# Kernel tuning notes

Hardware: AMD Instinct MI355X
Metric: run time of the kernel (lower is better)

Reference implementation:

```python
import jax, jax.numpy as jnp
import numpy as np

N = 50000          # nodes
E_RAW = 600000     # edges before self loops
FEAT = 64
HID = 64
HEADS = 4
NUM_SUBST = 32
NUM_GRAPHS = 128


def setup_inputs() -> dict:
    key = jax.random.key(0)
    ks = jax.random.split(key, 24)
    s = 0.05
    x = jax.random.normal(ks[0], (N, FEAT), jnp.float32)
    sids = jax.random.randint(ks[1], (N,), 0, NUM_SUBST)
    x = x.at[:, 5].set(sids.astype(jnp.float32))  # x[:,5] holds integer substructure ids
    edge_index = jax.random.randint(ks[2], (2, E_RAW), 0, N, dtype=jnp.int32)
    batch = jnp.sort(jax.random.randint(ks[3], (N,), 0, NUM_GRAPHS, dtype=jnp.int32))
    p = lambda i, shape: jax.random.normal(ks[i], shape, jnp.float32) * s
    return dict(
        x=x, edge_index=edge_index, batch=batch,
        # substructure attention MLP: Linear(FEAT,32) -> LeakyReLU(0.2) -> Linear(32,1)
        w_sa1=p(4, (FEAT, 32)), b_sa1=p(5, (32,)),
        w_sa2=p(6, (32, 1)), b_sa2=p(7, (1,)),
        # GATConv 1: in=FEAT+1, out=HID, heads=HEADS, concat
        W1=p(8, (FEAT + 1, HEADS * HID)), att_s1=p(9, (HEADS, HID)),
        att_d1=p(10, (HEADS, HID)), b1=p(11, (HEADS * HID,)),
        # GATConv 2: in=HEADS*HID, out=HID, heads=1
        W2=p(12, (HEADS * HID, HID)), att_s2=p(13, (1, HID)),
        att_d2=p(14, (1, HID)), b2=p(15, (HID,)),
        # prediction head
        Wp1=p(16, (HID, HID // 2)), bp1=p(17, (HID // 2,)),
        Wp2=p(18, (HID // 2, 1)), bp2=p(19, (1,)),
    )


def _gat_layer(h_in, src, dst, W, att_s, att_d, bias, n):
    heads, out_dim = att_s.shape
    h = (h_in @ W).reshape(n, heads, out_dim)            # [N, H, D]
    a_s = jnp.einsum('nhd,hd->nh', h, att_s)             # [N, H]
    a_d = jnp.einsum('nhd,hd->nh', h, att_d)
    e = jax.nn.leaky_relu(a_s[src] + a_d[dst], negative_slope=0.2)  # [E, H]
    m = jax.ops.segment_max(e, dst, num_segments=n)
    ex = jnp.exp(e - m[dst])
    denom = jax.ops.segment_sum(ex, dst, num_segments=n)
    alpha = ex / (denom[dst] + 1e-16)                    # segment softmax per dst node
    out = jax.ops.segment_sum(h[src] * alpha[..., None], dst, num_segments=n)
    return out.reshape(n, heads * out_dim) + bias        # concat heads + bias


def reference(x, edge_index, batch, w_sa1, b_sa1, w_sa2, b_sa2,
              W1, att_s1, att_d1, b1, W2, att_s2, att_d2, b2,
              Wp1, bp1, Wp2, bp2):
    n = x.shape[0]
    sid = jax.lax.stop_gradient(x[:, 5]).astype(jnp.int32)
    # segment mean of node features per substructure id (all NUM_SUBST ids present)
    cnt = jax.ops.segment_sum(jnp.ones((n,), x.dtype), sid, num_segments=NUM_SUBST)
    smean = jax.ops.segment_sum(x, sid, num_segments=NUM_SUBST) / jnp.maximum(cnt, 1.0)[:, None]
    logits = jax.nn.leaky_relu(smean @ w_sa1 + b_sa1, negative_slope=0.2) @ w_sa2 + b_sa2
    w = jax.nn.softmax(logits, axis=0)                   # [S, 1]
    atom_w = w[sid]                                      # broadcast back to atoms [N, 1]
    h = jnp.concatenate([x, atom_w], axis=1)             # [N, FEAT+1]
    # add_self_loops (gat2's remove+add self loops yields the same edge set)
    loops = jnp.arange(n, dtype=edge_index.dtype)
    src = jnp.concatenate([edge_index[0], loops])
    dst = jnp.concatenate([edge_index[1], loops])
    h = jax.nn.elu(_gat_layer(h, src, dst, W1, att_s1, att_d1, b1, n))
    h = _gat_layer(h, src, dst, W2, att_s2, att_d2, b2, n)
    g = jax.ops.segment_sum(h, batch, num_segments=NUM_GRAPHS)   # global_add_pool
    return jax.nn.elu(g @ Wp1 + bp1) @ Wp2 + bp2         # [NUM_GRAPHS, 1]
```

## Files before the change

### kernel.cpp

```cpp
#include <hip/hip_runtime.h>
#include <math.h>

#define N_NODES 50000
#define E_RAWN  600000
#define FEAT    64
#define HID     64
#define HEADS   4
#define NSUB    32
#define NGRAPH  128
#define NB_SCAN ((N_NODES + 255) / 256)
#define G2_NODES 128

__device__ __forceinline__ float leaky02(float v) { return v >= 0.f ? v : 0.2f * v; }
__device__ __forceinline__ float elu1(float v)    { return v > 0.f ? v : expm1f(v); }

__device__ __forceinline__ unsigned bf2pack(float a, float b) {
    unsigned ua = __float_as_uint(a), ub = __float_as_uint(b);
    ua = (ua + 0x7FFFu + ((ua >> 16) & 1u)) >> 16;
    ub = (ub + 0x7FFFu + ((ub >> 16) & 1u)) >> 16;
    return ua | (ub << 16);
}
__device__ __forceinline__ float bflo(unsigned p) { return __uint_as_float(p << 16); }
__device__ __forceinline__ float bfhi(unsigned p) { return __uint_as_float(p & 0xFFFF0000u); }
__device__ __forceinline__ float bfs(unsigned short v) { return __uint_as_float((unsigned)v << 16); }

__global__ void k_prep(const float* __restrict__ x,
                       float* __restrict__ ssum, float* __restrict__ scnt,
                       const int* __restrict__ dst, int* __restrict__ cnt) {
    int tid = threadIdx.x;
    if (blockIdx.x < 256) {
        __shared__ float lsum[NSUB * FEAT];
        __shared__ float lcnt[NSUB];
        for (int i = tid; i < NSUB * FEAT; i += 256) lsum[i] = 0.f;
        if (tid < NSUB) lcnt[tid] = 0.f;
        __syncthreads();
        const int total = N_NODES * FEAT;
        for (int idx = blockIdx.x * 256 + tid; idx < total; idx += 256 * 256) {
            int node = idx >> 6, f = idx & 63;
            int sid = (int)x[node * FEAT + 5];
            atomicAdd(&lsum[sid * FEAT + f], x[idx]);
            if (f == 0) atomicAdd(&lcnt[sid], 1.f);
        }
        __syncthreads();
        for (int i = tid; i < NSUB * FEAT; i += 256) atomicAdd(&ssum[i], lsum[i]);
        if (tid < NSUB) atomicAdd(&scnt[tid], lcnt[tid]);
    } else {
        for (int e = (blockIdx.x - 256) * 256 + tid; e < E_RAWN; e += 256 * 256)
            atomicAdd(&cnt[dst[e]], 1);
    }
}

__global__ void k_mlp_scan1(const int* __restrict__ cnt, int* __restrict__ offs, int* __restrict__ bsum,
                            const float* __restrict__ ssum, const float* __restrict__ scnt,
                            const float* __restrict__ w_sa1, const float* __restrict__ b_sa1,
                            const float* __restrict__ w_sa2, const float* __restrict__ b_sa2,
                            float* __restrict__ wsub) {
    int tid = threadIdx.x;
    if (blockIdx.x == NB_SCAN) {
        __shared__ float logits[NSUB];
        int s = tid;
        if (s < NSUB) {
            float c = fmaxf(scnt[s], 1.f);
            float sm[FEAT];
            for (int k = 0; k < FEAT; k++) sm[k] = ssum[s * FEAT + k] / c;
            float logit = b_sa2[0];
            for (int j = 0; j < 32; j++) {
                float hj = b_sa1[j];
                for (int k = 0; k < FEAT; k++) hj += sm[k] * w_sa1[k * 32 + j];
                hj = leaky02(hj);
                logit += hj * w_sa2[j];
            }
            logits[s] = logit;
        }
        __syncthreads();
        if (s < NSUB) {
            float m = -1e30f;
            for (int i = 0; i < NSUB; i++) m = fmaxf(m, logits[i]);
            float dsum = 0.f;
            for (int i = 0; i < NSUB; i++) dsum += expf(logits[i] - m);
            wsub[s] = expf(logits[s] - m) / dsum;
        }
        return;
    }
    __shared__ int sd[256];
    int i = blockIdx.x * 256 + tid;
    int v = (i < N_NODES) ? cnt[i] : 0;
    sd[tid] = v;
    for (int off = 1; off < 256; off <<= 1) {
        __syncthreads();
        int tv = (tid >= off) ? sd[tid - off] : 0;
        __syncthreads();
        sd[tid] += tv;
    }
    __syncthreads();
    if (i < N_NODES) offs[i] = sd[tid] - v;
    if (tid == 255) bsum[blockIdx.x] = sd[255];
}

__global__ __launch_bounds__(256) void k_gemm1(const float* __restrict__ x,
                                               const float* __restrict__ wsub,
                                               const float* __restrict__ W1,
                                               const float* __restrict__ att_s1,
                                               const float* __restrict__ att_d1,
                                               unsigned* __restrict__ h1b,
                                               float* __restrict__ as1, float* __restrict__ ad1) {
    __shared__ float xs[65][68];
    __shared__ float ws[16][260];
    int t = threadIdx.x;
    int gbase = blockIdx.x * 64;
    for (int idx = t; idx < 64 * 64; idx += 256) {
        int n = idx >> 6, f = idx & 63;
        int g = gbase + n;
        xs[f][n] = (g < N_NODES) ? x[(size_t)g * FEAT + f] : 0.f;
    }
    __syncthreads();
    if (t < 64) {
        int sid = (int)xs[5][t];
        xs[64][t] = wsub[sid & (NSUB - 1)];
    }

    int m = t & 31, q = t >> 5;
    int c0 = m * 8, q8 = q * 8;
    float accs[64];
    #pragma unroll
    for (int i = 0; i < 64; ++i) accs[i] = 0.f;

    for (int kc = 0; kc < 4; ++kc) {
        __syncthreads();
        #pragma unroll
        for (int s = 0; s < 16; ++s)
            ws[s][t] = W1[(size_t)(kc * 16 + s) * 256 + t];
        __syncthreads();
        #pragma unroll
        for (int kk = 0; kk < 16; ++kk) {
            float4 wa = *(const float4*)(&ws[kk][c0]);
            float4 wb = *(const float4*)(&ws[kk][c0 + 4]);
            float4 xa = *(const float4*)(&xs[kc * 16 + kk][q8]);
            float4 xb = *(const float4*)(&xs[kc * 16 + kk][q8 + 4]);
            float wv[8] = {wa.x, wa.y, wa.z, wa.w, wb.x, wb.y, wb.z, wb.w};
            float xv[8] = {xa.x, xa.y, xa.z, xa.w, xb.x, xb.y, xb.z, xb.w};
            #pragma unroll
            for (int c = 0; c < 8; ++c)
                #pragma unroll
                for (int j = 0; j < 8; ++j)
                    accs[c * 8 + j] += wv[c] * xv[j];
        }
    }
    {
        float4 wa = *(const float4*)(W1 + (size_t)64 * 256 + c0);
        float4 wb = *(const float4*)(W1 + (size_t)64 * 256 + c0 + 4);
        float4 xa = *(const float4*)(&xs[64][q8]);
        float4 xb = *(const float4*)(&xs[64][q8 + 4]);
        float wv[8] = {wa.x, wa.y, wa.z, wa.w, wb.x, wb.y, wb.z, wb.w};
        float xv[8] = {xa.x, xa.y, xa.z, xa.w, xb.x, xb.y, xb.z, xb.w};
        #pragma unroll
        for (int c = 0; c < 8; ++c)
            #pragma unroll
            for (int j = 0; j < 8; ++j)
                accs[c * 8 + j] += wv[c] * xv[j];
    }

    float atts[8], attd[8];
    #pragma unroll
    for (int c = 0; c < 8; ++c) { atts[c] = att_s1[c0 + c]; attd[c] = att_d1[c0 + c]; }
    int h = m >> 3;
    #pragma unroll
    for (int j = 0; j < 8; ++j) {
        int node = gbase + q8 + j;
        float ps = 0.f, pd = 0.f;
        #pragma unroll
        for (int c = 0; c < 8; ++c) { ps += accs[c * 8 + j] * atts[c]; pd += accs[c * 8 + j] * attd[c]; }
        ps += __shfl_xor(ps, 1, 64); pd += __shfl_xor(pd, 1, 64);
        ps += __shfl_xor(ps, 2, 64); pd += __shfl_xor(pd, 2, 64);
        ps += __shfl_xor(ps, 4, 64); pd += __shfl_xor(pd, 4, 64);
        if (node < N_NODES) {
            uint4 pk;
            pk.x = bf2pack(accs[0 * 8 + j], accs[1 * 8 + j]);
            pk.y = bf2pack(accs[2 * 8 + j], accs[3 * 8 + j]);
            pk.z = bf2pack(accs[4 * 8 + j], accs[5 * 8 + j]);
            pk.w = bf2pack(accs[6 * 8 + j], accs[7 * 8 + j]);
            *(uint4*)(h1b + (size_t)node * 128 + m * 4) = pk;
            if ((m & 7) == 0) { as1[node * 4 + h] = ps; ad1[node * 4 + h] = pd; }
        }
    }
}

__global__ void k_scan2(int* __restrict__ bsum, int nb) {
    __shared__ int sd[256];
    int tid = threadIdx.x;
    int v = (tid < nb) ? bsum[tid] : 0;
    sd[tid] = v;
    for (int off = 1; off < 256; off <<= 1) {
        __syncthreads();
        int tv = (tid >= off) ? sd[tid - off] : 0;
        __syncthreads();
        sd[tid] += tv;
    }
    __syncthreads();
    if (tid < nb) bsum[tid] = sd[tid] - v;
}

__global__ void k_scan3(int* __restrict__ offs, const int* __restrict__ bsum) {
    int i = blockIdx.x * 256 + threadIdx.x;
    if (i < N_NODES) offs[i] += bsum[blockIdx.x];
    if (blockIdx.x == 0 && threadIdx.x == 0) offs[N_NODES] = E_RAWN;
}

__global__ void k_scatter(const int* __restrict__ src, const int* __restrict__ dst,
                          const int* __restrict__ offs, int* __restrict__ cur,
                          int* __restrict__ esrc) {
    int e = blockIdx.x * blockDim.x + threadIdx.x;
    if (e < E_RAWN) {
        int d = dst[e];
        int pos = offs[d] + atomicAdd(&cur[d], 1);
        esrc[pos] = src[e];
    }
}

__global__ __launch_bounds__(256) void k_gat1(const unsigned* __restrict__ h1b,
                                              const float* __restrict__ as1,
                                              const float* __restrict__ ad1,
                                              const int* __restrict__ offs,
                                              const int* __restrict__ esrc,
                                              const float* __restrict__ b1,
                                              unsigned* __restrict__ hactb) {
    int wave = threadIdx.x >> 6, lane = threadIdx.x & 63;
    int i = blockIdx.x * 4 + wave;
    if (i >= N_NODES) return;
    int beg = offs[i], end = offs[i + 1];
    int h = lane >> 4;
    float adv = ad1[i * 4 + h];
    float w0 = __expf(leaky02(as1[i * 4 + h] + adv));
    uint2 hv = *(const uint2*)(h1b + (size_t)i * 128 + lane * 2);
    float4 acc = make_float4(w0 * bflo(hv.x), w0 * bfhi(hv.x), w0 * bflo(hv.y), w0 * bfhi(hv.y));
    float d = w0;
    int p = beg;
    for (; p + 3 < end; p += 4) {
        int s0 = esrc[p], s1 = esrc[p + 1], s2 = esrc[p + 2], s3 = esrc[p + 3];
        uint2 hA = *(const uint2*)(h1b + (size_t)s0 * 128 + lane * 2);
        uint2 hB = *(const uint2*)(h1b + (size_t)s1 * 128 + lane * 2);
        uint2 hC = *(const uint2*)(h1b + (size_t)s2 * 128 + lane * 2);
        uint2 hD = *(const uint2*)(h1b + (size_t)s3 * 128 + lane * 2);
        float a0 = as1[s0 * 4 + h], a1 = as1[s1 * 4 + h];
        float a2 = as1[s2 * 4 + h], a3 = as1[s3 * 4 + h];
        float wA = __expf(leaky02(a0 + adv));
        float wB = __expf(leaky02(a1 + adv));
        float wC = __expf(leaky02(a2 + adv));
        float wD = __expf(leaky02(a3 + adv));
        d += (wA + wB) + (wC + wD);
        acc.x += wA * bflo(hA.x) + wB * bflo(hB.x) + wC * bflo(hC.x) + wD * bflo(hD.x);
        acc.y += wA * bfhi(hA.x) + wB * bfhi(hB.x) + wC * bfhi(hC.x) + wD * bfhi(hD.x);
        acc.z += wA * bflo(hA.y) + wB * bflo(hB.y) + wC * bflo(hC.y) + wD * bflo(hD.y);
        acc.w += wA * bfhi(hA.y) + wB * bfhi(hB.y) + wC * bfhi(hC.y) + wD * bfhi(hD.y);
    }
    for (; p < end; ++p) {
        int s0 = esrc[p];
        uint2 hA = *(const uint2*)(h1b + (size_t)s0 * 128 + lane * 2);
        float wA = __expf(leaky02(as1[s0 * 4 + h] + adv));
        d += wA;
        acc.x += wA * bflo(hA.x);
        acc.y += wA * bfhi(hA.x);
        acc.z += wA * bflo(hA.y);
        acc.w += wA * bfhi(hA.y);
    }
    float inv = 1.f / (d + 1e-16f);
    float4 bb = *(const float4*)(b1 + lane * 4);
    float rx = elu1(acc.x * inv + bb.x);
    float ry = elu1(acc.y * inv + bb.y);
    float rz = elu1(acc.z * inv + bb.z);
    float rw = elu1(acc.w * inv + bb.w);
    uint2 pk;
    pk.x = bf2pack(rx, ry);
    pk.y = bf2pack(rz, rw);
    *(uint2*)(hactb + (size_t)i * 128 + lane * 2) = pk;
}

__global__ __launch_bounds__(256) void k_gemm2(const unsigned* __restrict__ hactb,
                                               const float* __restrict__ W2,
                                               const float* __restrict__ att_s2,
                                               const float* __restrict__ att_d2,
                                               unsigned short* __restrict__ h2b,
                                               float* __restrict__ as2, float* __restrict__ ad2) {
    __shared__ float hs[G2_NODES][68];
    int t = threadIdx.x;
    int gbase = blockIdx.x * G2_NODES;
    int m = t & 7, q = t >> 3;
    int c0 = m * 8, n0 = q * 4;
    float accs[32];
    #pragma unroll
    for (int i = 0; i < 32; ++i) accs[i] = 0.f;

    int sn = t >> 3;
    int sko = t & 7;

    for (int kc = 0; kc < 4; ++kc) {
        __syncthreads();
        #pragma unroll
        for (int r = 0; r < 4; ++r) {
            int n = sn + r * 32;
            int g = gbase + n;
            uint4 v = (g < N_NODES)
                ? *(const uint4*)(hactb + (size_t)g * 128 + kc * 32 + sko * 4)
                : make_uint4(0u, 0u, 0u, 0u);
            float4 lo = make_float4(bflo(v.x), bfhi(v.x), bflo(v.y), bfhi(v.y));
            float4 hi = make_float4(bflo(v.z), bfhi(v.z), bflo(v.w), bfhi(v.w));
            *(float4*)(&hs[n][sko * 8])     = lo;
            *(float4*)(&hs[n][sko * 8 + 4]) = hi;
        }
        __syncthreads();
        const float* Wc = W2 + (size_t)kc * 64 * 64;
        for (int kk = 0; kk < 16; ++kk) {
            float4 xv0 = *(const float4*)(&hs[n0 + 0][kk * 4]);
            float4 xv1 = *(const float4*)(&hs[n0 + 1][kk * 4]);
            float4 xv2 = *(const float4*)(&hs[n0 + 2][kk * 4]);
            float4 xv3 = *(const float4*)(&hs[n0 + 3][kk * 4]);
            const float* x0 = (const float*)&xv0;
            const float* x1 = (const float*)&xv1;
            const float* x2 = (const float*)&xv2;
            const float* x3 = (const float*)&xv3;
            #pragma unroll
            for (int jj = 0; jj < 4; ++jj) {
                int k = kk * 4 + jj;
                float4 wa = *(const float4*)(Wc + (size_t)k * 64 + c0);
                float4 wb = *(const float4*)(Wc + (size_t)k * 64 + c0 + 4);
                float wv[8] = {wa.x, wa.y, wa.z, wa.w, wb.x, wb.y, wb.z, wb.w};
                float xj[4] = {x0[jj], x1[jj], x2[jj], x3[jj]};
                #pragma unroll
                for (int c = 0; c < 8; ++c)
                    #pragma unroll
                    for (int j = 0; j < 4; ++j)
                        accs[c * 4 + j] += wv[c] * xj[j];
            }
        }
    }

    float atts[8], attd[8];
    #pragma unroll
    for (int c = 0; c < 8; ++c) { atts[c] = att_s2[c0 + c]; attd[c] = att_d2[c0 + c]; }
    #pragma unroll
    for (int j = 0; j < 4; ++j) {
        int node = gbase + n0 + j;
        float ps = 0.f, pd = 0.f;
        #pragma unroll
        for (int c = 0; c < 8; ++c) { ps += accs[c * 4 + j] * atts[c]; pd += accs[c * 4 + j] * attd[c]; }
        ps += __shfl_xor(ps, 1, 64); pd += __shfl_xor(pd, 1, 64);
        ps += __shfl_xor(ps, 2, 64); pd += __shfl_xor(pd, 2, 64);
        ps += __shfl_xor(ps, 4, 64); pd += __shfl_xor(pd, 4, 64);
        if (node < N_NODES) {
            uint4 pk;
            pk.x = bf2pack(accs[0 * 4 + j], accs[1 * 4 + j]);
            pk.y = bf2pack(accs[2 * 4 + j], accs[3 * 4 + j]);
            pk.z = bf2pack(accs[4 * 4 + j], accs[5 * 4 + j]);
            pk.w = bf2pack(accs[6 * 4 + j], accs[7 * 4 + j]);
            *(uint4*)(h2b + (size_t)node * 64 + c0) = pk;
            if (m == 0) { as2[node] = ps; ad2[node] = pd; }
        }
    }
}

__global__ __launch_bounds__(256) void k_gat2(const unsigned short* __restrict__ h2b,
                                              const float* __restrict__ as2,
                                              const float* __restrict__ ad2,
                                              const int* __restrict__ offs,
                                              const int* __restrict__ esrc,
                                              float* __restrict__ rbuf) {
    int wave = threadIdx.x >> 6, lane = threadIdx.x & 63;
    int i = blockIdx.x * 4 + wave;
    if (i >= N_NODES) return;
    int beg = offs[i], end = offs[i + 1];
    float adv = ad2[i];
    float w0 = __expf(leaky02(as2[i] + adv));
    float d = w0;
    float acc = w0 * bfs(h2b[(size_t)i * 64 + lane]);
    int p = beg;
    for (; p + 3 < end; p += 4) {
        int s0 = esrc[p], s1 = esrc[p + 1], s2 = esrc[p + 2], s3 = esrc[p + 3];
        float hA = bfs(h2b[(size_t)s0 * 64 + lane]);
        float hB = bfs(h2b[(size_t)s1 * 64 + lane]);
        float hC = bfs(h2b[(size_t)s2 * 64 + lane]);
        float hD = bfs(h2b[(size_t)s3 * 64 + lane]);
        float wA = __expf(leaky02(as2[s0] + adv));
        float wB = __expf(leaky02(as2[s1] + adv));
        float wC = __expf(leaky02(as2[s2] + adv));
        float wD = __expf(leaky02(as2[s3] + adv));
        d += (wA + wB) + (wC + wD);
        acc += wA * hA + wB * hB + wC * hC + wD * hD;
    }
    for (; p < end; ++p) {
        int s0 = esrc[p];
        float wA = __expf(leaky02(as2[s0] + adv));
        d += wA;
        acc += wA * bfs(h2b[(size_t)s0 * 64 + lane]);
    }
    rbuf[(size_t)i * 64 + lane] = acc / (d + 1e-16f);
}

__device__ __forceinline__ int lower_bound_i(const int* a, int n, int v) {
    int lo = 0, hi = n;
    while (lo < hi) { int mid = (lo + hi) >> 1; if (a[mid] < v) lo = mid + 1; else hi = mid; }
    return lo;
}

__global__ void k_pool_head(const float* __restrict__ rbuf, const int* __restrict__ batch,
                            const float* __restrict__ b2,
                            const float* __restrict__ Wp1, const float* __restrict__ bp1,
                            const float* __restrict__ Wp2, const float* __restrict__ bp2,
                            float* __restrict__ out) {
    __shared__ float red[4][64];
    __shared__ float tot[64];
    __shared__ float hred[32];
    int b = blockIdx.x;
    int lo = lower_bound_i(batch, N_NODES, b);
    int hi = lower_bound_i(batch, N_NODES, b + 1);
    int t = threadIdx.x;
    int c = t & 63, rg = t >> 6;
    float s = 0.f;
    for (int r = lo + rg; r < hi; r += 4) s += rbuf[(size_t)r * 64 + c];
    red[rg][c] = s;
    __syncthreads();
    if (rg == 0) tot[c] = red[0][c] + red[1][c] + red[2][c] + red[3][c] + (float)(hi - lo) * b2[c];
    __syncthreads();
    if (t < 32) {
        float hj = bp1[t];
        #pragma unroll
        for (int k = 0; k < 64; ++k) hj += tot[k] * Wp1[k * 32 + t];
        hred[t] = elu1(hj) * Wp2[t];
    }
    __syncthreads();
    if (t == 0) {
        float a = bp2[0];
        #pragma unroll
        for (int j = 0; j < 32; ++j) a += hred[j];
        out[b] = a;
    }
}

extern "C" void kernel_launch(void* const* d_in, const int* in_sizes, int n_in,
                              void* d_out, int out_size, void* d_ws, size_t ws_size,
                              hipStream_t stream) {
    const float* x      = (const float*)d_in[0];
    const int*   edge   = (const int*)d_in[1];
    const int*   batch  = (const int*)d_in[2];
    const float* w_sa1  = (const float*)d_in[3];
    const float* b_sa1  = (const float*)d_in[4];
    const float* w_sa2  = (const float*)d_in[5];
    const float* b_sa2  = (const float*)d_in[6];
    const float* W1     = (const float*)d_in[7];
    const float* att_s1 = (const float*)d_in[8];
    const float* att_d1 = (const float*)d_in[9];
    const float* b1     = (const float*)d_in[10];
    const float* W2     = (const float*)d_in[11];
    const float* att_s2 = (const float*)d_in[12];
    const float* att_d2 = (const float*)d_in[13];
    const float* b2     = (const float*)d_in[14];
    const float* Wp1    = (const float*)d_in[15];
    const float* bp1    = (const float*)d_in[16];
    const float* Wp2    = (const float*)d_in[17];
    const float* bp2    = (const float*)d_in[18];
    float* out = (float*)d_out;

    const int* e_src = edge;
    const int* e_dst = edge + E_RAWN;

    char* base = (char*)d_ws;
    size_t off = 0;
    auto alloc = [&](size_t bytes) -> void* {
        void* p = base + off;
        off = (off + bytes + 255) & ~(size_t)255;
        return p;
    };
    float* ssum   = (float*)alloc((NSUB * FEAT + NSUB) * 4);
    float* scnt   = ssum + NSUB * FEAT;
    float* wsub   = (float*)alloc(NSUB * 4);
    float* as1    = (float*)alloc((size_t)N_NODES * 4 * 4);
    float* ad1    = (float*)alloc((size_t)N_NODES * 4 * 4);
    float* as2    = (float*)alloc((size_t)N_NODES * 4);
    float* ad2    = (float*)alloc((size_t)N_NODES * 4);
    int*   counts = (int*)alloc((size_t)N_NODES * 2 * 4);
    int*   cursor = counts + N_NODES;
    int*   offs   = (int*)alloc((size_t)(N_NODES + 1) * 4);
    int*   bsum   = (int*)alloc(256 * 4);
    int*   esrc   = (int*)alloc((size_t)E_RAWN * 4);
    unsigned* h1b   = (unsigned*)alloc((size_t)N_NODES * 128 * 4);
    unsigned* hactb = (unsigned*)alloc((size_t)N_NODES * 128 * 4);
    unsigned short* h2b = (unsigned short*)alloc((size_t)N_NODES * 64 * 2);
    float* rbuf   = (float*)alloc((size_t)N_NODES * 64 * 4);

    (void)hipMemsetAsync(ssum,   0, (NSUB * FEAT + NSUB) * 4, stream);
    (void)hipMemsetAsync(counts, 0, (size_t)N_NODES * 2 * 4, stream);

    k_prep<<<512, 256, 0, stream>>>(x, ssum, scnt, e_dst, counts);
    k_mlp_scan1<<<NB_SCAN + 1, 256, 0, stream>>>(counts, offs, bsum,
                                                 ssum, scnt, w_sa1, b_sa1, w_sa2, b_sa2, wsub);
    k_gemm1<<<(N_NODES + 63) / 64, 256, 0, stream>>>(x, wsub, W1, att_s1, att_d1, h1b, as1, ad1);

    k_scan2<<<1, 256, 0, stream>>>(bsum, NB_SCAN);
    k_scan3<<<NB_SCAN, 256, 0, stream>>>(offs, bsum);
    k_scatter<<<(E_RAWN + 255) / 256, 256, 0, stream>>>(e_src, e_dst, offs, cursor, esrc);

    k_gat1<<<(N_NODES + 3) / 4, 256, 0, stream>>>(h1b, as1, ad1, offs, esrc, b1, hactb);
    k_gemm2<<<(N_NODES + G2_NODES - 1) / G2_NODES, 256, 0, stream>>>(hactb, W2, att_s2, att_d2, h2b, as2, ad2);
    k_gat2<<<(N_NODES + 3) / 4, 256, 0, stream>>>(h2b, as2, ad2, offs, esrc, rbuf);
    k_pool_head<<<NGRAPH, 256, 0, stream>>>(rbuf, batch, b2, Wp1, bp1, Wp2, bp2, out);
}
```

Baseline: 298.4 us.

## Fuse global pooling into GAT2 via atomics, merge scan kernels, single memset

Graph-level pooling moves into the second GAT aggregation kernel: each node atomically adds its output row into a per-graph accumulator, so the full per-node output buffer is no longer written and then re-read by the pooling kernel. The two-stage block-sum scan becomes one kernel, where each block reduces the preceding block sums itself, and the two memsets become one contiguous memset. The price is heavy float atomic contention on only 128×64 addresses, and summation order now varies from run to run.

```diff
diff --git a/kernel.cpp b/kernel.cpp
--- a/kernel.cpp
+++ b/kernel.cpp
@@ -185,25 +185,20 @@
     }
 }
 
-__global__ void k_scan2(int* __restrict__ bsum, int nb) {
+__global__ void k_scan3(int* __restrict__ offs, const int* __restrict__ bsum) {
     __shared__ int sd[256];
     int tid = threadIdx.x;
-    int v = (tid < nb) ? bsum[tid] : 0;
+    int v = (tid < (int)blockIdx.x && tid < NB_SCAN) ? bsum[tid] : 0;
     sd[tid] = v;
-    for (int off = 1; off < 256; off <<= 1) {
-        __syncthreads();
-        int tv = (tid >= off) ? sd[tid - off] : 0;
-        __syncthreads();
-        sd[tid] += tv;
-    }
     __syncthreads();
-    if (tid < nb) bsum[tid] = sd[tid] - v;
-}
-
-__global__ void k_scan3(int* __restrict__ offs, const int* __restrict__ bsum) {
-    int i = blockIdx.x * 256 + threadIdx.x;
-    if (i < N_NODES) offs[i] += bsum[blockIdx.x];
-    if (blockIdx.x == 0 && threadIdx.x == 0) offs[N_NODES] = E_RAWN;
+    for (int off = 128; off > 0; off >>= 1) {
+        if (tid < off) sd[tid] += sd[tid + off];
+        __syncthreads();
+    }
+    int prefix = sd[0];
+    int i = blockIdx.x * 256 + tid;
+    if (i < N_NODES) offs[i] += prefix;
+    if (blockIdx.x == 0 && tid == 0) offs[N_NODES] = E_RAWN;
 }
 
 __global__ void k_scatter(const int* __restrict__ src, const int* __restrict__ dst,
@@ -363,7 +358,8 @@
                                               const float* __restrict__ ad2,
                                               const int* __restrict__ offs,
                                               const int* __restrict__ esrc,
-                                              float* __restrict__ rbuf) {
+                                              const int* __restrict__ batch,
+                                              float* __restrict__ gpool) {
     int wave = threadIdx.x >> 6, lane = threadIdx.x & 63;
     int i = blockIdx.x * 4 + wave;
     if (i >= N_NODES) return;
@@ -392,7 +388,8 @@
         d += wA;
         acc += wA * bfs(h2b[(size_t)s0 * 64 + lane]);
     }
-    rbuf[(size_t)i * 64 + lane] = acc / (d + 1e-16f);
+    int b = batch[i];
+    atomicAdd(&gpool[(size_t)b * 64 + lane], acc / (d + 1e-16f));
 }
 
 __device__ __forceinline__ int lower_bound_i(const int* a, int n, int v) {
@@ -401,24 +398,18 @@
     return lo;
 }
 
-__global__ void k_pool_head(const float* __restrict__ rbuf, const int* __restrict__ batch,
-                            const float* __restrict__ b2,
-                            const float* __restrict__ Wp1, const float* __restrict__ bp1,
-                            const float* __restrict__ Wp2, const float* __restrict__ bp2,
-                            float* __restrict__ out) {
-    __shared__ float red[4][64];
+__global__ void k_head(const float* __restrict__ gpool, const int* __restrict__ batch,
+                       const float* __restrict__ b2,
+                       const float* __restrict__ Wp1, const float* __restrict__ bp1,
+                       const float* __restrict__ Wp2, const float* __restrict__ bp2,
+                       float* __restrict__ out) {
     __shared__ float tot[64];
     __shared__ float hred[32];
     int b = blockIdx.x;
+    int t = threadIdx.x;
     int lo = lower_bound_i(batch, N_NODES, b);
     int hi = lower_bound_i(batch, N_NODES, b + 1);
-    int t = threadIdx.x;
-    int c = t & 63, rg = t >> 6;
-    float s = 0.f;
-    for (int r = lo + rg; r < hi; r += 4) s += rbuf[(size_t)r * 64 + c];
-    red[rg][c] = s;
-    __syncthreads();
-    if (rg == 0) tot[c] = red[0][c] + red[1][c] + red[2][c] + red[3][c] + (float)(hi - lo) * b2[c];
+    tot[t] = gpool[(size_t)b * 64 + t] + (float)(hi - lo) * b2[t];
     __syncthreads();
     if (t < 32) {
         float hj = bp1[t];
@@ -471,35 +462,34 @@
     };
     float* ssum   = (float*)alloc((NSUB * FEAT + NSUB) * 4);
     float* scnt   = ssum + NSUB * FEAT;
+    int*   counts = (int*)alloc((size_t)N_NODES * 2 * 4);
+    int*   cursor = counts + N_NODES;
+    float* gpool  = (float*)alloc((size_t)NGRAPH * HID * 4);
+    size_t zero_bytes = off;
     float* wsub   = (float*)alloc(NSUB * 4);
     float* as1    = (float*)alloc((size_t)N_NODES * 4 * 4);
     float* ad1    = (float*)alloc((size_t)N_NODES * 4 * 4);
     float* as2    = (float*)alloc((size_t)N_NODES * 4);
     float* ad2    = (float*)alloc((size_t)N_NODES * 4);
-    int*   counts = (int*)alloc((size_t)N_NODES * 2 * 4);
-    int*   cursor = counts + N_NODES;
     int*   offs   = (int*)alloc((size_t)(N_NODES + 1) * 4);
     int*   bsum   = (int*)alloc(256 * 4);
     int*   esrc   = (int*)alloc((size_t)E_RAWN * 4);
     unsigned* h1b   = (unsigned*)alloc((size_t)N_NODES * 128 * 4);
     unsigned* hactb = (unsigned*)alloc((size_t)N_NODES * 128 * 4);
     unsigned short* h2b = (unsigned short*)alloc((size_t)N_NODES * 64 * 2);
-    float* rbuf   = (float*)alloc((size_t)N_NODES * 64 * 4);
-
-    (void)hipMemsetAsync(ssum,   0, (NSUB * FEAT + NSUB) * 4, stream);
-    (void)hipMemsetAsync(counts, 0, (size_t)N_NODES * 2 * 4, stream);
+
+    (void)hipMemsetAsync(base, 0, zero_bytes, stream);
 
     k_prep<<<512, 256, 0, stream>>>(x, ssum, scnt, e_dst, counts);
     k_mlp_scan1<<<NB_SCAN + 1, 256, 0, stream>>>(counts, offs, bsum,
                                                  ssum, scnt, w_sa1, b_sa1, w_sa2, b_sa2, wsub);
     k_gemm1<<<(N_NODES + 63) / 64, 256, 0, stream>>>(x, wsub, W1, att_s1, att_d1, h1b, as1, ad1);
 
-    k_scan2<<<1, 256, 0, stream>>>(bsum, NB_SCAN);
     k_scan3<<<NB_SCAN, 256, 0, stream>>>(offs, bsum);
     k_scatter<<<(E_RAWN + 255) / 256, 256, 0, stream>>>(e_src, e_dst, offs, cursor, esrc);
 
     k_gat1<<<(N_NODES + 3) / 4, 256, 0, stream>>>(h1b, as1, ad1, offs, esrc, b1, hactb);
     k_gemm2<<<(N_NODES + G2_NODES - 1) / G2_NODES, 256, 0, stream>>>(hactb, W2, att_s2, att_d2, h2b, as2, ad2);
-    k_gat2<<<(N_NODES + 3) / 4, 256, 0, stream>>>(h2b, as2, ad2, offs, esrc, rbuf);
-    k_pool_head<<<NGRAPH, 256, 0, stream>>>(rbuf, batch, b2, Wp1, bp1, Wp2, bp2, out);
-}
+    k_gat2<<<(N_NODES + 3) / 4, 256, 0, stream>>>(h2b, as2, ad2, offs, esrc, batch, gpool);
+    k_head<<<NGRAPH, 64, 0, stream>>>(gpool, batch, b2, Wp1, bp1, Wp2, bp2, out);
+}
```

After: 298.5 us. No clear change (+0.0%).

## Fuse scan stages into gemm1 launch, merge memsets, unroll gat2 by eight

Applied to the files above, without the earlier changes.

Drops the separate scan2 and scan3 launches. Extra blocks appended to the gemm1 grid each reduce the block sums below their own index and add that prefix to their slice of the offsets. The two memsets become one contiguous memset over a reordered workspace region, and the gat2 edge loop is unrolled from four to eight gathers per iteration to raise memory-level parallelism. This saves two kernel launches and one memset. The cost is redundant per-block reductions over bsum and higher register pressure in gat2.

```diff
diff --git a/kernel.cpp b/kernel.cpp
--- a/kernel.cpp
+++ b/kernel.cpp
@@ -10,6 +10,7 @@
 #define NGRAPH  128
 #define NB_SCAN ((N_NODES + 255) / 256)
 #define G2_NODES 128
+#define NBLK_G1 ((N_NODES + 63) / 64)
 
 __device__ __forceinline__ float leaky02(float v) { return v >= 0.f ? v : 0.2f * v; }
 __device__ __forceinline__ float elu1(float v)    { return v > 0.f ? v : expm1f(v); }
@@ -97,16 +98,33 @@
     if (tid == 255) bsum[blockIdx.x] = sd[255];
 }
 
-__global__ __launch_bounds__(256) void k_gemm1(const float* __restrict__ x,
-                                               const float* __restrict__ wsub,
-                                               const float* __restrict__ W1,
-                                               const float* __restrict__ att_s1,
-                                               const float* __restrict__ att_d1,
-                                               unsigned* __restrict__ h1b,
-                                               float* __restrict__ as1, float* __restrict__ ad1) {
+__global__ __launch_bounds__(256) void k_gemm1_scan3(const float* __restrict__ x,
+                                                     const float* __restrict__ wsub,
+                                                     const float* __restrict__ W1,
+                                                     const float* __restrict__ att_s1,
+                                                     const float* __restrict__ att_d1,
+                                                     unsigned* __restrict__ h1b,
+                                                     float* __restrict__ as1, float* __restrict__ ad1,
+                                                     int* __restrict__ offs, const int* __restrict__ bsum) {
+    int t = threadIdx.x;
+    if (blockIdx.x >= NBLK_G1) {
+        __shared__ int sd[256];
+        int b = blockIdx.x - NBLK_G1;
+        int v = (t < b && t < NB_SCAN) ? bsum[t] : 0;
+        sd[t] = v;
+        __syncthreads();
+        for (int off = 128; off > 0; off >>= 1) {
+            if (t < off) sd[t] += sd[t + off];
+            __syncthreads();
+        }
+        int prefix = sd[0];
+        int i = b * 256 + t;
+        if (i < N_NODES) offs[i] += prefix;
+        if (b == 0 && t == 0) offs[N_NODES] = E_RAWN;
+        return;
+    }
     __shared__ float xs[65][68];
     __shared__ float ws[16][260];
-    int t = threadIdx.x;
     int gbase = blockIdx.x * 64;
     for (int idx = t; idx < 64 * 64; idx += 256) {
         int n = idx >> 6, f = idx & 63;
@@ -183,27 +201,6 @@
             if ((m & 7) == 0) { as1[node * 4 + h] = ps; ad1[node * 4 + h] = pd; }
         }
     }
-}
-
-__global__ void k_scan2(int* __restrict__ bsum, int nb) {
-    __shared__ int sd[256];
-    int tid = threadIdx.x;
-    int v = (tid < nb) ? bsum[tid] : 0;
-    sd[tid] = v;
-    for (int off = 1; off < 256; off <<= 1) {
-        __syncthreads();
-        int tv = (tid >= off) ? sd[tid - off] : 0;
-        __syncthreads();
-        sd[tid] += tv;
-    }
-    __syncthreads();
-    if (tid < nb) bsum[tid] = sd[tid] - v;
-}
-
-__global__ void k_scan3(int* __restrict__ offs, const int* __restrict__ bsum) {
-    int i = blockIdx.x * 256 + threadIdx.x;
-    if (i < N_NODES) offs[i] += bsum[blockIdx.x];
-    if (blockIdx.x == 0 && threadIdx.x == 0) offs[N_NODES] = E_RAWN;
 }
 
 __global__ void k_scatter(const int* __restrict__ src, const int* __restrict__ dst,
@@ -373,18 +370,28 @@
     float d = w0;
     float acc = w0 * bfs(h2b[(size_t)i * 64 + lane]);
     int p = beg;
-    for (; p + 3 < end; p += 4) {
-        int s0 = esrc[p], s1 = esrc[p + 1], s2 = esrc[p + 2], s3 = esrc[p + 3];
+    for (; p + 7 < end; p += 8) {
+        int s0 = esrc[p],     s1 = esrc[p + 1], s2 = esrc[p + 2], s3 = esrc[p + 3];
+        int s4 = esrc[p + 4], s5 = esrc[p + 5], s6 = esrc[p + 6], s7 = esrc[p + 7];
         float hA = bfs(h2b[(size_t)s0 * 64 + lane]);
         float hB = bfs(h2b[(size_t)s1 * 64 + lane]);
         float hC = bfs(h2b[(size_t)s2 * 64 + lane]);
         float hD = bfs(h2b[(size_t)s3 * 64 + lane]);
+        float hE = bfs(h2b[(size_t)s4 * 64 + lane]);
+        float hF = bfs(h2b[(size_t)s5 * 64 + lane]);
+        float hG = bfs(h2b[(size_t)s6 * 64 + lane]);
+        float hH = bfs(h2b[(size_t)s7 * 64 + lane]);
         float wA = __expf(leaky02(as2[s0] + adv));
         float wB = __expf(leaky02(as2[s1] + adv));
         float wC = __expf(leaky02(as2[s2] + adv));
         float wD = __expf(leaky02(as2[s3] + adv));
-        d += (wA + wB) + (wC + wD);
-        acc += wA * hA + wB * hB + wC * hC + wD * hD;
+        float wE = __expf(leaky02(as2[s4] + adv));
+        float wF = __expf(leaky02(as2[s5] + adv));
+        float wG = __expf(leaky02(as2[s6] + adv));
+        float wH = __expf(leaky02(as2[s7] + adv));
+        d += ((wA + wB) + (wC + wD)) + ((wE + wF) + (wG + wH));
+        acc += (wA * hA + wB * hB + wC * hC + wD * hD)
+             + (wE * hE + wF * hF + wG * hG + wH * hH);
     }
     for (; p < end; ++p) {
         int s0 = esrc[p];
@@ -471,13 +478,14 @@
     };
     float* ssum   = (float*)alloc((NSUB * FEAT + NSUB) * 4);
     float* scnt   = ssum + NSUB * FEAT;
+    int*   counts = (int*)alloc((size_t)N_NODES * 2 * 4);
+    int*   cursor = counts + N_NODES;
+    size_t zero_bytes = off;
     float* wsub   = (float*)alloc(NSUB * 4);
     float* as1    = (float*)alloc((size_t)N_NODES * 4 * 4);
     float* ad1    = (float*)alloc((size_t)N_NODES * 4 * 4);
     float* as2    = (float*)alloc((size_t)N_NODES * 4);
     float* ad2    = (float*)alloc((size_t)N_NODES * 4);
-    int*   counts = (int*)alloc((size_t)N_NODES * 2 * 4);
-    int*   cursor = counts + N_NODES;
     int*   offs   = (int*)alloc((size_t)(N_NODES + 1) * 4);
     int*   bsum   = (int*)alloc(256 * 4);
     int*   esrc   = (int*)alloc((size_t)E_RAWN * 4);
@@ -486,16 +494,13 @@
     unsigned short* h2b = (unsigned short*)alloc((size_t)N_NODES * 64 * 2);
     float* rbuf   = (float*)alloc((size_t)N_NODES * 64 * 4);
 
-    (void)hipMemsetAsync(ssum,   0, (NSUB * FEAT + NSUB) * 4, stream);
-    (void)hipMemsetAsync(counts, 0, (size_t)N_NODES * 2 * 4, stream);
+    (void)hipMemsetAsync(base, 0, zero_bytes, stream);
 
     k_prep<<<512, 256, 0, stream>>>(x, ssum, scnt, e_dst, counts);
     k_mlp_scan1<<<NB_SCAN + 1, 256, 0, stream>>>(counts, offs, bsum,
                                                  ssum, scnt, w_sa1, b_sa1, w_sa2, b_sa2, wsub);
-    k_gemm1<<<(N_NODES + 63) / 64, 256, 0, stream>>>(x, wsub, W1, att_s1, att_d1, h1b, as1, ad1);
-
-    k_scan2<<<1, 256, 0, stream>>>(bsum, NB_SCAN);
-    k_scan3<<<NB_SCAN, 256, 0, stream>>>(offs, bsum);
+    k_gemm1_scan3<<<NBLK_G1 + NB_SCAN, 256, 0, stream>>>(x, wsub, W1, att_s1, att_d1,
+                                                         h1b, as1, ad1, offs, bsum);
     k_scatter<<<(E_RAWN + 255) / 256, 256, 0, stream>>>(e_src, e_dst, offs, cursor, esrc);
 
     k_gat1<<<(N_NODES + 3) / 4, 256, 0, stream>>>(h1b, as1, ad1, offs, esrc, b1, hactb);
```

Result: no change. 295.4 us (-1.0%).
